# Optimization experiments

Measured on AMD Instinct MI355X. Metric: run time of the kernel, lower is better.

The kernel has to match this reference:

```python
import jax, jax.numpy as jnp
import numpy as np

LRELU_GAIN = 2.0 ** 0.5  # util.lrelu_gain (assumed sqrt(2))
EPS = 1e-8


def upsample2_bilinear_ac(x):
    # F.upsample_bilinear == bilinear with align_corners=True, scale 2
    B, C, H, W = x.shape
    def lerp_axis(t, n, axis):
        c = jnp.arange(2 * n, dtype=jnp.float32) * (n - 1) / (2 * n - 1)
        i0 = jnp.floor(c).astype(jnp.int32)
        i1 = jnp.minimum(i0 + 1, n - 1)
        f = c - i0.astype(jnp.float32)
        a = jnp.take(t, i0, axis=axis)
        b = jnp.take(t, i1, axis=axis)
        shape = [1] * t.ndim
        shape[axis] = 2 * n
        f = f.reshape(shape)
        return a * (1.0 - f) + b * f
    x = lerp_axis(x, H, 2)
    x = lerp_axis(x, W, 3)
    return x


def conv1x1(x, weight, bias, gain):
    # Conv2dNormalizedLR with kernel_size=1: he = gain/sqrt(in)
    cin = weight.shape[1]
    he = gain / float(cin) ** 0.5
    y = jnp.einsum('bihw,oi->bohw', x, weight[:, :, 0, 0] * he)
    return y + bias[None, :, None, None]


def mod_conv3x3(x, weight, style, gain):
    # weight: [Cin, Cout, 3, 3]; style: [B, Cin]
    cin, cout, k, _ = weight.shape
    he = gain / float(cin * k * k) ** 0.5
    wmod = style[:, :, None, None, None] * (weight * he)[None]  # [B,Cin,Cout,k,k]
    # demodulation: normalize over (in, kh, kw) per out channel
    d = jax.lax.rsqrt(jnp.sum(wmod * wmod, axis=(1, 3, 4), keepdims=True) + EPS)
    wmod = wmod * d
    # conv_transpose2d(stride=1, pad=1, k=3) == conv2d with transposed+flipped kernel, pad=1
    kern = jnp.flip(jnp.transpose(wmod, (0, 2, 1, 3, 4)), axis=(3, 4))  # [B,Cout,Cin,k,k]
    def one(xb, kb):
        return jax.lax.conv_general_dilated(
            xb[None], kb, (1, 1), ((1, 1), (1, 1)),
            dimension_numbers=('NCHW', 'OIHW', 'NCHW'))[0]
    y = jax.vmap(one)(x, kern)
    return y * gain


def noise_affine(noise, w_s, b_s, w_b, b_b):
    # Baff*: 1x1 conv from 1 channel, gain=1 -> he=1
    ys = noise * w_s[None, :, 0, None, 0, None][:, :, :, 0] if False else noise * w_s[:, 0, 0, 0][None, :, None, None] + b_s[None, :, None, None]
    yb = noise * w_b[:, 0, 0, 0][None, :, None, None] + b_b[None, :, None, None]
    return ys, yb


def block_forward(x, w, noise1, noise2, conv1_w, bias1, conv2_w, bias2,
                  Aaff1_w, Aaff1_b, Aaff2_w, Aaff2_b,
                  Baff1s_w, Baff1s_b, Baff1b_w, Baff1b_b,
                  Baff2s_w, Baff2s_b, Baff2b_w, Baff2b_b,
                  rgb_w, rgb_b):
    x = upsample2_bilinear_ac(x)
    style1 = conv1x1(w, Aaff1_w, Aaff1_b, 1.0)[:, :, 0, 0]  # [B, Cin]
    x = mod_conv3x3(x, conv1_w, style1, LRELU_GAIN)
    ys, yb = noise_affine(noise1, Baff1s_w, Baff1s_b, Baff1b_w, Baff1b_b)
    x = x * ys + yb + bias1
    x = jax.nn.leaky_relu(x, 0.2)
    style2 = conv1x1(w, Aaff2_w, Aaff2_b, 1.0)[:, :, 0, 0]
    x = mod_conv3x3(x, conv2_w, style2, LRELU_GAIN)
    ys, yb = noise_affine(noise2, Baff2s_w, Baff2s_b, Baff2b_w, Baff2b_b)
    x = x * ys + yb + bias2
    x = jax.nn.leaky_relu(x, 0.2)
    rgb = conv1x1(x, rgb_w, rgb_b, 0.03)
    return x, rgb


def setup_inputs() -> dict:
    key = jax.random.key(0)
    ks = jax.random.split(key, 20)
    B, Cin, Cout, Wd, H, W = 8, 512, 512, 512, 32, 32
    inp = {
        'x': jax.random.normal(ks[0], (B, Cin, H, W), jnp.float32),
        'w': jax.random.normal(ks[1], (B, Wd, 1, 1), jnp.float32),
        'noise1': jax.random.normal(ks[2], (B, 1, 2 * H, 2 * W), jnp.float32),
        'noise2': jax.random.normal(ks[3], (B, 1, 2 * H, 2 * W), jnp.float32),
        'conv1_w': jax.random.normal(ks[4], (Cin, Cout, 3, 3), jnp.float32),
        'bias1': jnp.zeros((1, Cout, 1, 1), jnp.float32),
        'conv2_w': jax.random.normal(ks[5], (Cout, Cout, 3, 3), jnp.float32),
        'bias2': jnp.zeros((1, Cout, 1, 1), jnp.float32),
        'Aaff1_w': jax.random.normal(ks[6], (Cin, Wd, 1, 1), jnp.float32),
        'Aaff1_b': jnp.zeros((Cin,), jnp.float32),
        'Aaff2_w': jax.random.normal(ks[7], (Cout, Wd, 1, 1), jnp.float32),
        'Aaff2_b': jnp.zeros((Cout,), jnp.float32),
        'Baff1s_w': jax.random.normal(ks[8], (Cout, 1, 1, 1), jnp.float32) * 0.1,
        'Baff1s_b': jnp.ones((Cout,), jnp.float32),
        'Baff1b_w': jax.random.normal(ks[9], (Cout, 1, 1, 1), jnp.float32) * 0.1,
        'Baff1b_b': jnp.zeros((Cout,), jnp.float32),
        'Baff2s_w': jax.random.normal(ks[10], (Cout, 1, 1, 1), jnp.float32) * 0.1,
        'Baff2s_b': jnp.ones((Cout,), jnp.float32),
        'Baff2b_w': jax.random.normal(ks[11], (Cout, 1, 1, 1), jnp.float32) * 0.1,
        'Baff2b_b': jnp.zeros((Cout,), jnp.float32),
        'rgb_w': jax.random.normal(ks[12], (3, Cout, 1, 1), jnp.float32),
        'rgb_b': jnp.zeros((3,), jnp.float32),
    }
    return inp


def reference(x, w, noise1, noise2, conv1_w, bias1, conv2_w, bias2,
              Aaff1_w, Aaff1_b, Aaff2_w, Aaff2_b,
              Baff1s_w, Baff1s_b, Baff1b_w, Baff1b_b,
              Baff2s_w, Baff2s_b, Baff2b_w, Baff2b_b,
              rgb_w, rgb_b):
    return block_forward(x, w, noise1, noise2, conv1_w, bias1, conv2_w, bias2,
                         Aaff1_w, Aaff1_b, Aaff2_w, Aaff2_b,
                         Baff1s_w, Baff1s_b, Baff1b_w, Baff1b_b,
                         Baff2s_w, Baff2s_b, Baff2b_w, Baff2b_b,
                         rgb_w, rgb_b)
```

## Files before the change

### kernel.cpp

```cpp
#include <hip/hip_runtime.h>
#include <hip/hip_bf16.h>

#define BB 8
#define CC 512
#define HO 64
#define HP 66
#define NPIX (BB*HO*HO)

typedef float f32x4 __attribute__((ext_vector_type(4)));
typedef __bf16 bf16x8 __attribute__((ext_vector_type(8)));
using bf16 = __hip_bfloat16;

__device__ __forceinline__ void gload16(const void* g, void* l) {
    __builtin_amdgcn_global_load_lds((const __attribute__((address_space(1))) void*)g,
                                     (__attribute__((address_space(3))) void*)l, 16, 0, 0);
}

__device__ __forceinline__ float waveRedSum(float v) {
    #pragma unroll
    for (int off = 32; off; off >>= 1) v += __shfl_down(v, off);
    return v;
}

__global__ void prep_weights(const float* __restrict__ Wsrc, float* __restrict__ S2ho,
                             bf16* __restrict__ keffT, float he) {
    int t = blockIdx.x * blockDim.x + threadIdx.x;
    int i = t & (CC-1), o = t >> 9;
    const float* wp = Wsrc + (i*CC + o)*9;
    float v[9]; float s2 = 0.f;
    #pragma unroll
    for (int k = 0; k < 9; ++k) { v[k] = wp[k] * he; s2 += v[k]*v[k]; }
    S2ho[o*CC + i] = s2;
    #pragma unroll
    for (int tp = 0; tp < 9; ++tp) keffT[(tp*CC + o)*CC + i] = (bf16)v[8 - tp];
}

__global__ void style_kernel(const float* __restrict__ w,
                             const float* __restrict__ A1, const float* __restrict__ A1b,
                             const float* __restrict__ A2, const float* __restrict__ A2b,
                             float* __restrict__ s1, float* __restrict__ s2) {
    int wid = (blockIdx.x * blockDim.x + threadIdx.x) >> 6;
    int lane = threadIdx.x & 63;
    int set = wid >= BB*CC; int rem = set ? wid - BB*CC : wid;
    int b = rem >> 9, i = rem & (CC-1);
    const float* A = set ? A2 : A1;
    const float* wb = w + b*CC;
    float sum = 0.f;
    for (int d = lane; d < CC; d += 64) sum += wb[d] * A[i*CC + d];
    sum = waveRedSum(sum);
    if (lane == 0) {
        float r = sum * 0.04419417382415922f + (set ? A2b : A1b)[i];
        (set ? s2 : s1)[b*CC + i] = r;
    }
}

__global__ void demod_kernel(const float* __restrict__ s1, const float* __restrict__ S21,
                             const float* __restrict__ s2, const float* __restrict__ S22,
                             float* __restrict__ dg1, float* __restrict__ dg2, float gain) {
    int wid = (blockIdx.x * blockDim.x + threadIdx.x) >> 6;
    int lane = threadIdx.x & 63;
    int set = wid >= BB*CC; int rem = set ? wid - BB*CC : wid;
    int b = rem >> 9, o = rem & (CC-1);
    const float* st = (set ? s2 : s1) + b*CC;
    const float* S2 = (set ? S22 : S21) + o*CC;
    float sum = 0.f;
    for (int i = lane; i < CC; i += 64) { float sv = st[i]; sum += sv*sv*S2[i]; }
    sum = waveRedSum(sum);
    if (lane == 0) (set ? dg2 : dg1)[b*CC + o] = gain * rsqrtf(sum + 1e-8f);
}

__global__ void upsample_mod(const float* __restrict__ x, const float* __restrict__ s1,
                             bf16* __restrict__ xs1) {
    __shared__ float usl[16][CC];
    int blk = blockIdx.x;
    int i = threadIdx.x;
    int b = blk >> 10, rem = blk & 1023, p = rem >> 4, q0 = (rem & 15) << 2;
    const float scale = 31.0f / 63.0f;
    float chf = p * scale; int h0 = (int)chf; float fh = chf - h0; int h1 = min(h0 + 1, 31);
    int wa = min(((int)(q0 * scale)) & ~3, 24);
    const float* xb = x + ((size_t)(b*CC + i) << 10);
    f32x4 r00 = *(const f32x4*)(xb + (h0 << 5) + wa);
    f32x4 r01 = *(const f32x4*)(xb + (h0 << 5) + wa + 4);
    f32x4 r10 = *(const f32x4*)(xb + (h1 << 5) + wa);
    f32x4 r11 = *(const f32x4*)(xb + (h1 << 5) + wa + 4);
    #pragma unroll
    for (int k = 0; k < 4; ++k) {
        usl[k][i] = r00[k]; usl[4 + k][i] = r01[k];
        usl[8 + k][i] = r10[k]; usl[12 + k][i] = r11[k];
    }
    float sv = s1[b*CC + i];
    #pragma unroll
    for (int dq = 0; dq < 4; ++dq) {
        int q = q0 + dq;
        float cwf = q * scale; int w0 = (int)cwf; float fw = cwf - w0;
        int i0 = w0 - wa, i1 = min(w0 + 1, 31) - wa;
        float v00 = usl[i0][i], v01 = usl[i1][i];
        float v10 = usl[8 + i0][i], v11 = usl[8 + i1][i];
        float va = v00*(1.f-fh) + v10*fh;
        float vb = v01*(1.f-fh) + v11*fh;
        float v  = (va*(1.f-fw) + vb*fw) * sv;
        xs1[(((b*HP) + p + 1)*HP + (q + 1))*CC + i] = (bf16)v;
    }
}

#define VM4 asm volatile("s_waitcnt vmcnt(4)" ::: "memory")
#define BARR do { asm volatile("" ::: "memory"); __builtin_amdgcn_s_barrier(); \
                  asm volatile("" ::: "memory"); } while (0)

#define STAGE_A(d, h, U) do { \
    gload16((U) + aThr + (h)*(HP*1024),                 ldsA + (d)*32768 + (h)*16384); \
    gload16((U) + aThr + (h)*(HP*1024) + 2*(HP*1024),   ldsA + (d)*32768 + (h)*16384 + 8192); \
} while (0)

#define STAGE_B(d, h, U) do { \
    gload16((U) + bThr + (h)*32768,                     ldsB + (d)*32768 + (h)*16384); \
    gload16((U) + bThr + (h)*32768 + 131072,            ldsB + (d)*32768 + (h)*16384 + 8192); \
} while (0)

#define LOAD_A(d, fh) do { \
    _Pragma("unroll") \
    for (int fmq = 0; fmq < 4; ++fmq) { \
        afr[fmq][0] = *(const bf16x8*)(aRd + (d)*32768 + (fh)*16384 + fmq*2048 + swz0); \
        afr[fmq][1] = *(const bf16x8*)(aRd + (d)*32768 + (fh)*16384 + fmq*2048 + swz1); \
    } } while (0)

#define LOAD_B(d, nh) do { \
    _Pragma("unroll") \
    for (int fnq = 0; fnq < 2; ++fnq) { \
        bfr[fnq][0] = *(const bf16x8*)(bRd + (d)*32768 + (nh)*16384 + fnq*2048 + swz0); \
        bfr[fnq][1] = *(const bf16x8*)(bRd + (d)*32768 + (nh)*16384 + fnq*2048 + swz1); \
    } } while (0)

#define QUAD(fh, nh) do { \
    __builtin_amdgcn_s_setprio(1); \
    _Pragma("unroll") \
    for (int kc = 0; kc < 2; ++kc) \
    { _Pragma("unroll") \
      for (int fmq = 0; fmq < 4; ++fmq) \
      { _Pragma("unroll") \
        for (int fnq = 0; fnq < 2; ++fnq) \
            acc[(fh)*4+fmq][(nh)*2+fnq] = __builtin_amdgcn_mfma_f32_16x16x32_bf16( \
                afr[fmq][kc], bfr[fnq][kc], acc[(fh)*4+fmq][(nh)*2+fnq], 0, 0, 0); } } \
    __builtin_amdgcn_s_setprio(0); } while (0)

#define PHGROUP(dc, sd, Au, Bu, doStage) do { \
    if (doStage) STAGE_A(sd, 0, Au); \
    LOAD_A(dc, 0); LOAD_B(dc, 0); \
    QUAD(0, 0); \
    VM4; BARR; \
    if (doStage) STAGE_B(sd, 0, Bu); \
    LOAD_A(dc, 1); \
    QUAD(1, 0); \
    VM4; BARR; \
    if (doStage) STAGE_A(sd, 1, Au); \
    LOAD_B(dc, 1); \
    QUAD(1, 1); \
    BARR; \
    if (doStage) STAGE_B(sd, 1, Bu); \
    LOAD_A(dc, 0); \
    QUAD(0, 1); \
    VM4; BARR; \
} while (0)

template<int PHASE>
__global__ __launch_bounds__(512, 2) void conv_gemm(
    const bf16* __restrict__ xs, const bf16* __restrict__ keffT,
    const float* __restrict__ dg, const float* __restrict__ noise,
    const float* __restrict__ nsw, const float* __restrict__ nsb,
    const float* __restrict__ nbw, const float* __restrict__ nbb,
    const float* __restrict__ biasv, const float* __restrict__ stnext,
    bf16* __restrict__ outb, float* __restrict__ outf) {
    __shared__ __attribute__((aligned(16))) bf16 As[32768];
    __shared__ __attribute__((aligned(16))) bf16 Bs[32768];
    const int tid = threadIdx.x;
    const int wave = tid >> 6, lane = tid & 63;
    const int tileId = ((blockIdx.x & 7) << 5) + (blockIdx.x >> 3);
    const int mtile = tileId >> 1, ntile = tileId & 1;
    const int m0 = mtile << 8, n0 = ntile << 8;
    const int b  = m0 >> 12;
    const int p0 = (m0 & 4095) >> 6;
    const int wm = wave >> 2, wn = wave & 3;
    const int l15 = lane & 15;

    const int srcSwz = (((tid & 7) ^ ((tid >> 3) & 7)) << 4);
    const int aThr = ((tid >> 3) << 10) + srcSwz;
    const int bThr = (((tid >> 8) & 1) << 16) + (((tid >> 3) & 31) << 10) + srcSwz;
    char* const ldsA = (char*)As + tid*16;
    char* const ldsB = (char*)Bs + tid*16;

    const char* const aRd = (const char*)As + (((wm << 6) + l15) << 7);
    const char* const bRd = (const char*)Bs + (((wn << 5) + l15) << 7);
    const int swz0 = (((lane >> 4)    ) ^ (lane & 7)) << 4;
    const int swz1 = (((lane >> 4) | 4) ^ (lane & 7)) << 4;

    f32x4 acc[8][4];
    #pragma unroll
    for (int i_ = 0; i_ < 8; ++i_)
        #pragma unroll
        for (int j_ = 0; j_ < 4; ++j_) acc[i_][j_] = f32x4{0.f, 0.f, 0.f, 0.f};
    bf16x8 afr[4][2], bfr[2][2];

    auto abase = [&](int st) -> const char* {
        int t = st >> 3; int dh = (t*11) >> 5; int dw = t - dh*3;
        return (const char*)xs + ((size_t)((b*HP + p0 + dh)*HP + dw) << 10) + ((st & 7) << 7);
    };
    auto bbase = [&](int st) -> const char* {
        int t = st >> 3;
        return (const char*)keffT + ((size_t)(t*CC + n0) << 10) + ((st & 7) << 7);
    };

    {
        const char* a0 = abase(0); const char* b0 = bbase(0);
        STAGE_A(0, 0, a0); STAGE_B(0, 0, b0);
        STAGE_A(0, 1, a0); STAGE_B(0, 1, b0);
        VM4; BARR;
    }

    #pragma unroll 1
    for (int it = 0; it < 36; ++it) {
        const char* a1 = abase(2*it + 1);
        const char* b1 = bbase(2*it + 1);
        const bool more = (it < 35);
        const char* a2 = abase(2*it + 2);
        const char* b2 = bbase(2*it + 2);
        PHGROUP(0, 1, a1, b1, true);
        PHGROUP(1, 0, a2, b2, more);
    }

    const float* dgb = dg + b*CC;
    int nIdx[4]; float pdg[4], pnsw[4], pnsb[4], pnbw[4], pnbb[4], pbias[4], pst[4];
    #pragma unroll
    for (int fn = 0; fn < 4; ++fn) {
        int n = n0 + (wn << 6) + (fn << 4) + l15;
        nIdx[fn] = n;
        pdg[fn] = dgb[n]; pnsw[fn] = nsw[n]; pnsb[fn] = nsb[n];
        pnbw[fn] = nbw[n]; pnbb[fn] = nbb[n]; pbias[fn] = biasv[n];
        if (PHASE == 1) pst[fn] = stnext[b*CC + n]; else pst[fn] = 0.f;
    }
    #pragma unroll
    for (int fm = 0; fm < 8; ++fm) {
        #pragma unroll
        for (int r = 0; r < 4; ++r) {
            int mloc = m0 + (wm << 7) + (fm << 4) + ((lane >> 4) << 2) + r;
            float ns = noise[mloc];
            int prow = (mloc & 4095) >> 6, qcol = mloc & 63;
            #pragma unroll
            for (int fn = 0; fn < 4; ++fn) {
                float v = acc[fm][fn][r] * pdg[fn];
                v = v * (ns*pnsw[fn] + pnsb[fn]) + (ns*pnbw[fn] + pnbb[fn]) + pbias[fn];
                v = fmaxf(v, 0.2f*v);
                if (PHASE == 1) {
                    outb[(((b*HP) + prow + 1)*HP + (qcol + 1))*CC + nIdx[fn]] =
                        (bf16)(v * pst[fn]);
                } else {
                    outf[((b*CC + nIdx[fn]) << 12) + (mloc & 4095)] = v;
                }
            }
        }
    }
}

__global__ void rgb_kernel(const float* __restrict__ xf, const float* __restrict__ rgbw,
                           const float* __restrict__ rgbb, float* __restrict__ out) {
    __shared__ float red[3][4][64];
    int tid = threadIdx.x;
    int wv = tid >> 6, ln = tid & 63;
    int pix = blockIdx.x * 64 + ln;
    int b = pix >> 12, rem = pix & 4095;
    const float* xb = xf + (((size_t)b*CC) << 12) + rem;
    float a0 = 0.f, a1 = 0.f, a2 = 0.f;
    int o0 = wv << 7;
    #pragma unroll 8
    for (int o = o0; o < o0 + 128; ++o) {
        float xv = xb[(size_t)o << 12];
        a0 += xv * rgbw[o]; a1 += xv * rgbw[CC+o]; a2 += xv * rgbw[2*CC+o];
    }
    red[0][wv][ln] = a0; red[1][wv][ln] = a1; red[2][wv][ln] = a2;
    __syncthreads();
    if (wv == 0) {
        const float he = 0.03f * 0.04419417382415922f;
        #pragma unroll
        for (int c = 0; c < 3; ++c) {
            float s = red[c][0][ln] + red[c][1][ln] + red[c][2][ln] + red[c][3][ln];
            out[(b*3+c)*4096 + rem] = s*he + rgbb[c];
        }
    }
}

extern "C" void kernel_launch(void* const* d_in, const int* in_sizes, int n_in,
                              void* d_out, int out_size, void* d_ws, size_t ws_size,
                              hipStream_t stream) {
    const float* x      = (const float*)d_in[0];
    const float* w      = (const float*)d_in[1];
    const float* noise1 = (const float*)d_in[2];
    const float* noise2 = (const float*)d_in[3];
    const float* conv1w = (const float*)d_in[4];
    const float* bias1  = (const float*)d_in[5];
    const float* conv2w = (const float*)d_in[6];
    const float* bias2  = (const float*)d_in[7];
    const float* A1w = (const float*)d_in[8];
    const float* A1b = (const float*)d_in[9];
    const float* A2w = (const float*)d_in[10];
    const float* A2b = (const float*)d_in[11];
    const float* B1sw = (const float*)d_in[12];
    const float* B1sb = (const float*)d_in[13];
    const float* B1bw = (const float*)d_in[14];
    const float* B1bb = (const float*)d_in[15];
    const float* B2sw = (const float*)d_in[16];
    const float* B2sb = (const float*)d_in[17];
    const float* B2bw = (const float*)d_in[18];
    const float* B2bb = (const float*)d_in[19];
    const float* rgbw = (const float*)d_in[20];
    const float* rgbb = (const float*)d_in[21];

    char* ws = (char*)d_ws;
    size_t off = 0;
    auto alloc = [&](size_t bytes) { char* p = ws + off; off += (bytes + 255) & ~(size_t)255; return p; };
    const size_t xsBytes = (size_t)BB*HP*HP*CC*2;
    bf16* xs1 = (bf16*)alloc(xsBytes);
    bf16* xs2 = (bf16*)alloc(xsBytes);
    bf16* kT1 = (bf16*)alloc((size_t)9*CC*CC*2);
    bf16* kT2 = (bf16*)alloc((size_t)9*CC*CC*2);
    float* S21 = (float*)alloc((size_t)CC*CC*4);
    float* S22 = (float*)alloc((size_t)CC*CC*4);
    float* s1  = (float*)alloc(BB*CC*4);
    float* s2  = (float*)alloc(BB*CC*4);
    float* dg1 = (float*)alloc(BB*CC*4);
    float* dg2 = (float*)alloc(BB*CC*4);

    float* outx   = (float*)d_out;
    float* outrgb = outx + (size_t)BB*CC*HO*HO;

    hipMemsetAsync(xs1, 0, xsBytes, stream);
    hipMemsetAsync(xs2, 0, xsBytes, stream);

    const float gain = 1.41421356237309515f;
    const float he = gain / sqrtf(512.f * 9.f);
    prep_weights<<<CC*CC/256, 256, 0, stream>>>(conv1w, S21, kT1, he);
    prep_weights<<<CC*CC/256, 256, 0, stream>>>(conv2w, S22, kT2, he);
    style_kernel<<<2*BB*CC/4, 256, 0, stream>>>(w, A1w, A1b, A2w, A2b, s1, s2);
    demod_kernel<<<2*BB*CC/4, 256, 0, stream>>>(s1, S21, s2, S22, dg1, dg2, gain);
    upsample_mod<<<BB*HO*16, CC, 0, stream>>>(x, s1, xs1);
    conv_gemm<1><<<(NPIX/256)*(CC/256), 512, 0, stream>>>(
        xs1, kT1, dg1, noise1, B1sw, B1sb, B1bw, B1bb, bias1, s2, xs2, nullptr);
    conv_gemm<2><<<(NPIX/256)*(CC/256), 512, 0, stream>>>(
        xs2, kT2, dg2, noise2, B2sw, B2sb, B2bw, B2bb, bias2, nullptr, nullptr, outx);
    rgb_kernel<<<NPIX/64, 256, 0, stream>>>(outx, rgbw, rgbb, outrgb);
}
```

Measured before the change: 393.0 us.

## Restructure conv GEMM main loop into deeper prefetch schedule with explicit waitcnts

Rewrites the double-buffered main loop of the implicit-GEMM conv kernel. Each half-stage is now split into four MFMA quadrants in a new order, and the A tile for the stage after next is staged early into the current buffer. Explicit lgkmcnt/vmcnt waits and sched_barriers pin the interleaving of LDS reads, global-to-LDS loads and MFMAs. B fragments are double-registered so both halves stay live. The aim is to hide global load latency and reduce barrier stalls, at the cost of more registers, more barriers per step, and a higher risk of LDS buffer-reuse hazards.

New measurement: 384.3 us. -2.2%, faster.

```diff
diff --git a/kernel.cpp b/kernel.cpp
--- a/kernel.cpp
+++ b/kernel.cpp
@@ -103,9 +103,10 @@
     }
 }
 
-#define VM4 asm volatile("s_waitcnt vmcnt(4)" ::: "memory")
-#define BARR do { asm volatile("" ::: "memory"); __builtin_amdgcn_s_barrier(); \
-                  asm volatile("" ::: "memory"); } while (0)
+#define SB  __builtin_amdgcn_sched_barrier(0)
+#define BAR __builtin_amdgcn_s_barrier()
+#define VMC(n)  asm volatile("s_waitcnt vmcnt(" #n ")" ::: "memory")
+#define LGKM(n) asm volatile("s_waitcnt lgkmcnt(" #n ")" ::: "memory")
 
 #define STAGE_A(d, h, U) do { \
     gload16((U) + aThr + (h)*(HP*1024),                 ldsA + (d)*32768 + (h)*16384); \
@@ -127,8 +128,8 @@
 #define LOAD_B(d, nh) do { \
     _Pragma("unroll") \
     for (int fnq = 0; fnq < 2; ++fnq) { \
-        bfr[fnq][0] = *(const bf16x8*)(bRd + (d)*32768 + (nh)*16384 + fnq*2048 + swz0); \
-        bfr[fnq][1] = *(const bf16x8*)(bRd + (d)*32768 + (nh)*16384 + fnq*2048 + swz1); \
+        bfr[nh][fnq][0] = *(const bf16x8*)(bRd + (d)*32768 + (nh)*16384 + fnq*2048 + swz0); \
+        bfr[nh][fnq][1] = *(const bf16x8*)(bRd + (d)*32768 + (nh)*16384 + fnq*2048 + swz1); \
     } } while (0)
 
 #define QUAD(fh, nh) do { \
@@ -140,26 +141,35 @@
       { _Pragma("unroll") \
         for (int fnq = 0; fnq < 2; ++fnq) \
             acc[(fh)*4+fmq][(nh)*2+fnq] = __builtin_amdgcn_mfma_f32_16x16x32_bf16( \
-                afr[fmq][kc], bfr[fnq][kc], acc[(fh)*4+fmq][(nh)*2+fnq], 0, 0, 0); } } \
+                afr[fmq][kc], bfr[nh][fnq][kc], acc[(fh)*4+fmq][(nh)*2+fnq], 0, 0, 0); } } \
     __builtin_amdgcn_s_setprio(0); } while (0)
 
-#define PHGROUP(dc, sd, Au, Bu, doStage) do { \
-    if (doStage) STAGE_A(sd, 0, Au); \
-    LOAD_A(dc, 0); LOAD_B(dc, 0); \
+#define PHSTEP(cur, nxt, aN1, bN1, aN2, g1, g3) do { \
+     \
+    LOAD_A(cur, 0); \
+    LOAD_B(cur, 0); \
+    if (g1) STAGE_B(nxt, 0, bN1); \
+    LGKM(8); SB; BAR; LGKM(0); SB; \
     QUAD(0, 0); \
-    VM4; BARR; \
-    if (doStage) STAGE_B(sd, 0, Bu); \
-    LOAD_A(dc, 1); \
+    VMC(4); SB; BAR; SB; \
+     \
+    LOAD_B(cur, 1); \
+    if (g1) STAGE_B(nxt, 1, bN1); \
+    SB; BAR; LGKM(0); SB; \
+    QUAD(0, 1); \
+    SB; BAR; SB; \
+     \
+    LOAD_A(cur, 1); \
+    if (g1) STAGE_A(nxt, 1, aN1); \
+    SB; BAR; LGKM(0); SB; \
+    QUAD(1, 1); \
+    SB; BAR; SB; \
+     \
+    if (g3) STAGE_A(cur, 0, aN2); \
+    SB; BAR; SB; \
     QUAD(1, 0); \
-    VM4; BARR; \
-    if (doStage) STAGE_A(sd, 1, Au); \
-    LOAD_B(dc, 1); \
-    QUAD(1, 1); \
-    BARR; \
-    if (doStage) STAGE_B(sd, 1, Bu); \
-    LOAD_A(dc, 0); \
-    QUAD(0, 1); \
-    VM4; BARR; \
+    if (g3) { VMC(6); } else { VMC(0); } \
+    SB; BAR; SB; \
 } while (0)
 
 template<int PHASE>
@@ -198,7 +208,7 @@
     for (int i_ = 0; i_ < 8; ++i_)
         #pragma unroll
         for (int j_ = 0; j_ < 4; ++j_) acc[i_][j_] = f32x4{0.f, 0.f, 0.f, 0.f};
-    bf16x8 afr[4][2], bfr[2][2];
+    bf16x8 afr[4][2], bfr[2][2][2];
 
     auto abase = [&](int st) -> const char* {
         int t = st >> 3; int dh = (t*11) >> 5; int dw = t - dh*3;
@@ -210,21 +220,23 @@
     };
 
     {
-        const char* a0 = abase(0); const char* b0 = bbase(0);
-        STAGE_A(0, 0, a0); STAGE_B(0, 0, b0);
-        STAGE_A(0, 1, a0); STAGE_B(0, 1, b0);
-        VM4; BARR;
+        const char* a0 = abase(0); const char* b0 = bbase(0); const char* a1 = abase(1);
+        STAGE_A(0, 0, a0);
+        STAGE_B(0, 0, b0);
+        STAGE_B(0, 1, b0);
+        STAGE_A(0, 1, a0);
+        STAGE_A(1, 0, a1);
+        VMC(6); SB; BAR; SB;
     }
 
     #pragma unroll 1
     for (int it = 0; it < 36; ++it) {
-        const char* a1 = abase(2*it + 1);
-        const char* b1 = bbase(2*it + 1);
         const bool more = (it < 35);
-        const char* a2 = abase(2*it + 2);
-        const char* b2 = bbase(2*it + 2);
-        PHGROUP(0, 1, a1, b1, true);
-        PHGROUP(1, 0, a2, b2, more);
+        const char* aE = abase(2*it + 1); const char* bE = bbase(2*it + 1);
+        const char* aO = abase(2*it + 2); const char* bO = bbase(2*it + 2);
+        const char* aO2 = abase(2*it + 3);
+        PHSTEP(0, 1, aE, bE, aO,  true, more);
+        PHSTEP(1, 0, aO, bO, aO2, more, more);
     }
 
     const float* dgb = dg + b*CC;
```

## Retile conv GEMM to 256x128 with triple-buffered LDS pipeline

Applied to the files above, without the earlier changes.

Output tiles in the implicit-GEMM conv kernels shrink from 256x256 to 256x128, doubling the grid to 512 blocks and halving per-wave accumulators. The LDS pipeline moves from double to triple buffering, so each K step loads its fragments and stages the next-next stage before the MFMA bursts. It uses fewer barriers and vmcnt waits per K step. The goal is better load/compute overlap and more blocks across the CUs, at the cost of more A-operand reloads from global memory and occupancy reduced to one block per CU.

After: 413.1 us. 5.1% more time.

```diff
diff --git a/kernel.cpp b/kernel.cpp
--- a/kernel.cpp
+++ b/kernel.cpp
@@ -103,102 +103,100 @@
     }
 }
 
-#define VM4 asm volatile("s_waitcnt vmcnt(4)" ::: "memory")
 #define BARR do { asm volatile("" ::: "memory"); __builtin_amdgcn_s_barrier(); \
                   asm volatile("" ::: "memory"); } while (0)
+#define VMC(n) asm volatile("s_waitcnt vmcnt(" #n ")" ::: "memory")
+#define HPB (HP*1024)
 
 #define STAGE_A(d, h, U) do { \
-    gload16((U) + aThr + (h)*(HP*1024),                 ldsA + (d)*32768 + (h)*16384); \
-    gload16((U) + aThr + (h)*(HP*1024) + 2*(HP*1024),   ldsA + (d)*32768 + (h)*16384 + 8192); \
+    gload16((U) + aThr + (2*(h)  )*HPB, (char*)As + (d)*32768 + (h)*16384 + tid*16); \
+    gload16((U) + aThr + (2*(h)+1)*HPB, (char*)As + (d)*32768 + (h)*16384 + tid*16 + 8192); \
 } while (0)
 
-#define STAGE_B(d, h, U) do { \
-    gload16((U) + bThr + (h)*32768,                     ldsB + (d)*32768 + (h)*16384); \
-    gload16((U) + bThr + (h)*32768 + 131072,            ldsB + (d)*32768 + (h)*16384 + 8192); \
+#define STAGE_B(d, U) do { \
+    gload16((U) + bThr,         (char*)Bs + (d)*16384 + tid*16); \
+    gload16((U) + bThr + 65536, (char*)Bs + (d)*16384 + tid*16 + 8192); \
 } while (0)
 
 #define LOAD_A(d, fh) do { \
     _Pragma("unroll") \
-    for (int fmq = 0; fmq < 4; ++fmq) { \
-        afr[fmq][0] = *(const bf16x8*)(aRd + (d)*32768 + (fh)*16384 + fmq*2048 + swz0); \
-        afr[fmq][1] = *(const bf16x8*)(aRd + (d)*32768 + (fh)*16384 + fmq*2048 + swz1); \
+    for (int fmq = 0; fmq < 2; ++fmq) { \
+        afr[fmq][0] = *(const bf16x8*)(aRd + (d)*32768 + (fh)*4096 + fmq*2048 + swz0); \
+        afr[fmq][1] = *(const bf16x8*)(aRd + (d)*32768 + (fh)*4096 + fmq*2048 + swz1); \
     } } while (0)
 
 #define LOAD_B(d, nh) do { \
     _Pragma("unroll") \
     for (int fnq = 0; fnq < 2; ++fnq) { \
-        bfr[fnq][0] = *(const bf16x8*)(bRd + (d)*32768 + (nh)*16384 + fnq*2048 + swz0); \
-        bfr[fnq][1] = *(const bf16x8*)(bRd + (d)*32768 + (nh)*16384 + fnq*2048 + swz1); \
+        bfr[nh][fnq][0] = *(const bf16x8*)(bRd + (d)*16384 + (nh)*4096 + fnq*2048 + swz0); \
+        bfr[nh][fnq][1] = *(const bf16x8*)(bRd + (d)*16384 + (nh)*4096 + fnq*2048 + swz1); \
     } } while (0)
 
 #define QUAD(fh, nh) do { \
-    __builtin_amdgcn_s_setprio(1); \
     _Pragma("unroll") \
     for (int kc = 0; kc < 2; ++kc) \
     { _Pragma("unroll") \
-      for (int fmq = 0; fmq < 4; ++fmq) \
+      for (int fmq = 0; fmq < 2; ++fmq) \
       { _Pragma("unroll") \
         for (int fnq = 0; fnq < 2; ++fnq) \
-            acc[(fh)*4+fmq][(nh)*2+fnq] = __builtin_amdgcn_mfma_f32_16x16x32_bf16( \
-                afr[fmq][kc], bfr[fnq][kc], acc[(fh)*4+fmq][(nh)*2+fnq], 0, 0, 0); } } \
-    __builtin_amdgcn_s_setprio(0); } while (0)
-
-#define PHGROUP(dc, sd, Au, Bu, doStage) do { \
-    if (doStage) STAGE_A(sd, 0, Au); \
-    LOAD_A(dc, 0); LOAD_B(dc, 0); \
-    QUAD(0, 0); \
-    VM4; BARR; \
-    if (doStage) STAGE_B(sd, 0, Bu); \
-    LOAD_A(dc, 1); \
-    QUAD(1, 0); \
-    VM4; BARR; \
-    if (doStage) STAGE_A(sd, 1, Au); \
-    LOAD_B(dc, 1); \
-    QUAD(1, 1); \
+            acc[(fh)*2+fmq][(nh)*2+fnq] = __builtin_amdgcn_mfma_f32_16x16x32_bf16( \
+                afr[fmq][kc], bfr[nh][fnq][kc], acc[(fh)*2+fmq][(nh)*2+fnq], 0, 0, 0); } } \
+    } while (0)
+
+#define KSTEP(cur, stg, aN, bN, DOST, VMODE) do { \
+    LOAD_A(cur, 0); LOAD_B(cur, 0); LOAD_B(cur, 1); \
+    if (DOST) { STAGE_A(stg, 0, aN); STAGE_A(stg, 1, aN); } \
     BARR; \
-    if (doStage) STAGE_B(sd, 1, Bu); \
-    LOAD_A(dc, 0); \
-    QUAD(0, 1); \
-    VM4; BARR; \
+    __builtin_amdgcn_s_setprio(1); \
+    QUAD(0, 0); QUAD(0, 1); \
+    __builtin_amdgcn_s_setprio(0); \
+    BARR; \
+    LOAD_A(cur, 1); \
+    if (DOST) STAGE_B(stg, bN); \
+    BARR; \
+    __builtin_amdgcn_s_setprio(1); \
+    QUAD(1, 1); QUAD(1, 0); \
+    __builtin_amdgcn_s_setprio(0); \
+    if (VMODE == 2) { VMC(6); } else if (VMODE == 1) { VMC(0); } \
+    BARR; \
 } while (0)
 
 template<int PHASE>
-__global__ __launch_bounds__(512, 2) void conv_gemm(
+__global__ __launch_bounds__(512, 1) void conv_gemm(
     const bf16* __restrict__ xs, const bf16* __restrict__ keffT,
     const float* __restrict__ dg, const float* __restrict__ noise,
     const float* __restrict__ nsw, const float* __restrict__ nsb,
     const float* __restrict__ nbw, const float* __restrict__ nbb,
     const float* __restrict__ biasv, const float* __restrict__ stnext,
     bf16* __restrict__ outb, float* __restrict__ outf) {
-    __shared__ __attribute__((aligned(16))) bf16 As[32768];
-    __shared__ __attribute__((aligned(16))) bf16 Bs[32768];
+    __shared__ __attribute__((aligned(16))) bf16 As[49152];
+    __shared__ __attribute__((aligned(16))) bf16 Bs[24576];
     const int tid = threadIdx.x;
     const int wave = tid >> 6, lane = tid & 63;
-    const int tileId = ((blockIdx.x & 7) << 5) + (blockIdx.x >> 3);
-    const int mtile = tileId >> 1, ntile = tileId & 1;
-    const int m0 = mtile << 8, n0 = ntile << 8;
+    const int tileId = ((blockIdx.x & 7) << 6) + (blockIdx.x >> 3);
+    const int mtile = tileId >> 2, ntile = tileId & 3;
+    const int m0 = mtile << 8, n0 = ntile << 7;
     const int b  = m0 >> 12;
     const int p0 = (m0 & 4095) >> 6;
-    const int wm = wave >> 2, wn = wave & 3;
+    const int wm = wave >> 1, wn = wave & 1;
     const int l15 = lane & 15;
 
-    const int srcSwz = (((tid & 7) ^ ((tid >> 3) & 7)) << 4);
-    const int aThr = ((tid >> 3) << 10) + srcSwz;
-    const int bThr = (((tid >> 8) & 1) << 16) + (((tid >> 3) & 31) << 10) + srcSwz;
-    char* const ldsA = (char*)As + tid*16;
-    char* const ldsB = (char*)Bs + tid*16;
-
-    const char* const aRd = (const char*)As + (((wm << 6) + l15) << 7);
-    const char* const bRd = (const char*)Bs + (((wn << 5) + l15) << 7);
+    const int preswz = (((tid & 7) ^ ((tid >> 3) & 7)) << 4);
+    const int aThr = ((tid >> 3) << 10) + preswz;
+    const int bThr = ((tid >> 3) << 10) + preswz;
+
+    const char* const aRd = (const char*)As + ((wm >> 1) * 16384)
+                          + ((((wm & 1) << 6) + l15) << 7);
+    const char* const bRd = (const char*)Bs + (((wn << 6) + l15) << 7);
     const int swz0 = (((lane >> 4)    ) ^ (lane & 7)) << 4;
     const int swz1 = (((lane >> 4) | 4) ^ (lane & 7)) << 4;
 
-    f32x4 acc[8][4];
-    #pragma unroll
-    for (int i_ = 0; i_ < 8; ++i_)
+    f32x4 acc[4][4];
+    #pragma unroll
+    for (int i_ = 0; i_ < 4; ++i_)
         #pragma unroll
         for (int j_ = 0; j_ < 4; ++j_) acc[i_][j_] = f32x4{0.f, 0.f, 0.f, 0.f};
-    bf16x8 afr[4][2], bfr[2][2];
+    bf16x8 afr[2][2], bfr[2][2][2];
 
     auto abase = [&](int st) -> const char* {
         int t = st >> 3; int dh = (t*11) >> 5; int dw = t - dh*3;
@@ -211,20 +209,23 @@
 
     {
         const char* a0 = abase(0); const char* b0 = bbase(0);
-        STAGE_A(0, 0, a0); STAGE_B(0, 0, b0);
-        STAGE_A(0, 1, a0); STAGE_B(0, 1, b0);
-        VM4; BARR;
+        const char* a1 = abase(1); const char* b1 = bbase(1);
+        STAGE_A(0, 0, a0); STAGE_A(0, 1, a0); STAGE_B(0, b0);
+        STAGE_A(1, 0, a1); STAGE_A(1, 1, a1); STAGE_B(1, b1);
+        VMC(6); BARR;
     }
 
     #pragma unroll 1
-    for (int it = 0; it < 36; ++it) {
-        const char* a1 = abase(2*it + 1);
-        const char* b1 = bbase(2*it + 1);
-        const bool more = (it < 35);
-        const char* a2 = abase(2*it + 2);
-        const char* b2 = bbase(2*it + 2);
-        PHGROUP(0, 1, a1, b1, true);
-        PHGROUP(1, 0, a2, b2, more);
+    for (int g = 0; g < 24; ++g) {
+        const int s = 3*g;
+        KSTEP(0, 2, abase(s+2), bbase(s+2), true, 2);
+        if (g < 23) {
+            KSTEP(1, 0, abase(s+3), bbase(s+3), true, 2);
+            KSTEP(2, 1, abase(s+4), bbase(s+4), true, 2);
+        } else {
+            KSTEP(1, 0, abase(0), bbase(0), false, 1);
+            KSTEP(2, 1, abase(0), bbase(0), false, 0);
+        }
     }
 
     const float* dgb = dg + b*CC;
@@ -238,10 +239,10 @@
         if (PHASE == 1) pst[fn] = stnext[b*CC + n]; else pst[fn] = 0.f;
     }
     #pragma unroll
-    for (int fm = 0; fm < 8; ++fm) {
+    for (int fm = 0; fm < 4; ++fm) {
         #pragma unroll
         for (int r = 0; r < 4; ++r) {
-            int mloc = m0 + (wm << 7) + (fm << 4) + ((lane >> 4) << 2) + r;
+            int mloc = m0 + (wm << 6) + (fm << 4) + ((lane >> 4) << 2) + r;
             float ns = noise[mloc];
             int prow = (mloc & 4095) >> 6, qcol = mloc & 63;
             #pragma unroll
@@ -341,9 +342,9 @@
     style_kernel<<<2*BB*CC/4, 256, 0, stream>>>(w, A1w, A1b, A2w, A2b, s1, s2);
     demod_kernel<<<2*BB*CC/4, 256, 0, stream>>>(s1, S21, s2, S22, dg1, dg2, gain);
     upsample_mod<<<BB*HO*16, CC, 0, stream>>>(x, s1, xs1);
-    conv_gemm<1><<<(NPIX/256)*(CC/256), 512, 0, stream>>>(
+    conv_gemm<1><<<(NPIX/256)*(CC/128), 512, 0, stream>>>(
         xs1, kT1, dg1, noise1, B1sw, B1sb, B1bw, B1bb, bias1, s2, xs2, nullptr);
-    conv_gemm<2><<<(NPIX/256)*(CC/256), 512, 0, stream>>>(
+    conv_gemm<2><<<(NPIX/256)*(CC/128), 512, 0, stream>>>(
         xs2, kT2, dg2, noise2, B2sw, B2sb, B2bw, B2bb, bias2, nullptr, nullptr, outx);
     rgb_kernel<<<NPIX/64, 256, 0, stream>>>(outx, rgbw, rgbb, outrgb);
 }
```
